# Kernel tuning notes

Hardware: AMD Instinct MI355X
Metric: run time of the kernel (lower is better)

Reference implementation:

```python
import jax, jax.numpy as jnp
import numpy as np
import math

B, S, D_MODEL, N_HEAD, D_HEAD, D_FFN = 1, 2048, 1024, 16, 64, 4096
EPS = 1e-6


def setup_inputs() -> dict:
    key = jax.random.key(0)
    ks = jax.random.split(key, 10)
    scale = 0.02
    x = jax.random.normal(ks[0], (B, S, D_MODEL), dtype=jnp.float32)
    # RoPE frequencies: freqs_cis[s, i] = exp(1j * s * theta_i), theta_i = 10000^{-2i/d_head}
    half = D_HEAD // 2
    inv_freq = 1.0 / (10000.0 ** (jnp.arange(0, half, dtype=jnp.float32) * 2.0 / D_HEAD))
    angles = jnp.arange(S, dtype=jnp.float32)[:, None] * inv_freq[None, :]  # [S, half]
    freqs_cos = jnp.cos(angles)
    freqs_sin = jnp.sin(angles)
    wq = jax.random.normal(ks[1], (D_MODEL, N_HEAD * D_HEAD), dtype=jnp.float32) * scale
    wk = jax.random.normal(ks[2], (D_MODEL, N_HEAD * D_HEAD), dtype=jnp.float32) * scale
    wv = jax.random.normal(ks[3], (D_MODEL, N_HEAD * D_HEAD), dtype=jnp.float32) * scale
    wo = jax.random.normal(ks[4], (N_HEAD * D_HEAD, D_MODEL), dtype=jnp.float32) * scale
    w1 = jax.random.normal(ks[5], (D_MODEL, D_FFN), dtype=jnp.float32) * scale
    w2 = jax.random.normal(ks[6], (D_FFN, D_MODEL), dtype=jnp.float32) * scale
    w3 = jax.random.normal(ks[7], (D_MODEL, D_FFN), dtype=jnp.float32) * scale
    attn_norm_w = jnp.ones((D_MODEL,), dtype=jnp.float32)
    ffn_norm_w = jnp.ones((D_MODEL,), dtype=jnp.float32)
    return {"x": x, "freqs_cos": freqs_cos, "freqs_sin": freqs_sin,
            "wq": wq, "wk": wk, "wv": wv, "wo": wo,
            "w1": w1, "w2": w2, "w3": w3,
            "attn_norm_w": attn_norm_w, "ffn_norm_w": ffn_norm_w}


def _rmsnorm(x, w):
    xf = x.astype(jnp.float32)
    inv = jax.lax.rsqrt(jnp.mean(xf * xf, axis=-1, keepdims=True) + EPS)
    return (xf * inv).astype(x.dtype) * w


def _rope(t, cos, sin):
    # t: [B, S, H, D]; treat last dim as interleaved (even, odd) complex pairs
    b, s, h, d = t.shape
    tr = t.astype(jnp.float32).reshape(b, s, h, d // 2, 2)
    te, to = tr[..., 0], tr[..., 1]
    c = cos[None, :, None, :]
    sn = sin[None, :, None, :]
    out = jnp.stack([te * c - to * sn, te * sn + to * c], axis=-1)
    return out.reshape(b, s, h, d).astype(t.dtype)


def reference(x, freqs_cos, freqs_sin, wq, wk, wv, wo, w1, w2, w3, attn_norm_w, ffn_norm_w):
    bsz, seqlen, _ = x.shape
    # --- attention sub-block ---
    hin = _rmsnorm(x, attn_norm_w)
    q = (hin @ wq).reshape(bsz, seqlen, N_HEAD, D_HEAD)
    k = (hin @ wk).reshape(bsz, seqlen, N_HEAD, D_HEAD)
    v = (hin @ wv).reshape(bsz, seqlen, N_HEAD, D_HEAD)
    q = _rope(q, freqs_cos, freqs_sin)
    k = _rope(k, freqs_cos, freqs_sin)
    # [B, H, S, S] scores, softmax in fp32 (no causal mask in original)
    scores = jnp.einsum('bqhd,bkhd->bhqk', q, k) / math.sqrt(D_HEAD)
    probs = jax.nn.softmax(scores.astype(jnp.float32), axis=-1).astype(q.dtype)
    attn = jnp.einsum('bhqk,bkhd->bqhd', probs, v).reshape(bsz, seqlen, N_HEAD * D_HEAD)
    h = x + attn @ wo
    # --- SwiGLU FFN sub-block ---
    f = _rmsnorm(h, ffn_norm_w)
    ffn = (jax.nn.silu(f @ w1) * (f @ w3)) @ w2
    return h + ffn
```

## Files before the change

kernel.cpp:

```cpp
#include <hip/hip_runtime.h>
#include <stdint.h>
#include <stddef.h>

using bf16x8 = __attribute__((ext_vector_type(8))) __bf16;
using f32x4  = __attribute__((ext_vector_type(4))) float;
using f32x16 = __attribute__((ext_vector_type(16))) float;

__device__ __forceinline__ float bf2f(unsigned short u) {
  union { unsigned int i; float f; } v; v.i = ((unsigned int)u) << 16; return v.f;
}
__device__ __forceinline__ unsigned short f2bf(float f) {
  union { float f; unsigned int i; } v; v.f = f;
  unsigned int r = v.i + 0x7fffu + ((v.i >> 16) & 1u);
  return (unsigned short)(r >> 16);
}
__device__ __forceinline__ unsigned short f2bf_trunc(float f) {
  union { float f; unsigned int i; } v; v.f = f;
  return (unsigned short)(v.i >> 16);
}
__device__ __forceinline__ unsigned int pk_trunc(float a, float b) {
  union { float f; unsigned int i; } x, y; x.f = a; y.f = b;
  return (x.i >> 16) | (y.i & 0xffff0000u);
}
__device__ __forceinline__ bf16x8 mk_bf16x8(unsigned int a, unsigned int b,
                                            unsigned int c, unsigned int d) {
  union { unsigned int u[4]; bf16x8 v; } x;
  x.u[0] = a; x.u[1] = b; x.u[2] = c; x.u[3] = d; return x.v;
}
__device__ __forceinline__ void async16(const void* g, void* l) {
  __builtin_amdgcn_global_load_lds(
      (const __attribute__((address_space(1))) unsigned int*)g,
      (__attribute__((address_space(3))) unsigned int*)l, 16, 0, 0);
}

#define S_LEN 2048
#define DMODEL 1024
#define NHEAD 16
#define DHEAD 64
#define DFFN 4096

struct T4 {
  const float *s0, *s1, *s2, *s3;
  unsigned short *d0, *d1, *d2, *d3;
};
__global__ __launch_bounds__(256) void transpose4_k(T4 j) {
  const float* in = blockIdx.z == 0 ? j.s0 : blockIdx.z == 1 ? j.s1 : blockIdx.z == 2 ? j.s2 : j.s3;
  unsigned short* out = blockIdx.z == 0 ? j.d0 : blockIdx.z == 1 ? j.d1 : blockIdx.z == 2 ? j.d2 : j.d3;
  __shared__ unsigned short tile[32][33];
  const int tx = threadIdx.x & 31;
  const int ty = threadIdx.x >> 5;
  const int bc = blockIdx.x * 32;
  const int br = blockIdx.y * 32;
#pragma unroll
  for (int i = 0; i < 4; ++i)
    tile[ty + i * 8][tx] = f2bf(in[(size_t)(br + ty + i * 8) * 1024 + bc + tx]);
  __syncthreads();
#pragma unroll
  for (int i = 0; i < 4; ++i)
    out[(size_t)(bc + ty + i * 8) * 1024 + br + tx] = tile[tx][ty + i * 8];
}

__global__ __launch_bounds__(256) void transpose13_k(
    const float* __restrict__ w1, const float* __restrict__ w3,
    unsigned short* __restrict__ out) {
  const float* in = blockIdx.z ? w3 : w1;
  const int rb = blockIdx.z * 32;
  __shared__ unsigned short tile[32][33];
  const int tx = threadIdx.x & 31;
  const int ty = threadIdx.x >> 5;
  const int bc = blockIdx.x * 32;
  const int br = blockIdx.y * 32;
#pragma unroll
  for (int i = 0; i < 4; ++i)
    tile[ty + i * 8][tx] = f2bf(in[(size_t)(br + ty + i * 8) * 4096 + bc + tx]);
  __syncthreads();
#pragma unroll
  for (int i = 0; i < 4; ++i) {
    int c = bc + ty + i * 8;
    int dest = (c >> 5) * 64 + rb + (c & 31);
    out[(size_t)dest * 1024 + br + tx] = tile[tx][ty + i * 8];
  }
}

__global__ __launch_bounds__(256) void transpose_w2_k(
    const float* __restrict__ in, unsigned short* __restrict__ out) {
  __shared__ unsigned short tile[32][33];
  const int tx = threadIdx.x & 31;
  const int ty = threadIdx.x >> 5;
  const int bc = blockIdx.x * 32;
  const int br = blockIdx.y * 32;
#pragma unroll
  for (int i = 0; i < 4; ++i)
    tile[ty + i * 8][tx] = f2bf(in[(size_t)(br + ty + i * 8) * 1024 + bc + tx]);
  __syncthreads();
#pragma unroll
  for (int i = 0; i < 4; ++i)
    out[(size_t)(bc + ty + i * 8) * 4096 + br + tx] = tile[tx][ty + i * 8];
}

__global__ __launch_bounds__(256) void vtrans_k(
    const unsigned short* __restrict__ QKV, unsigned short* __restrict__ VtG) {
  __shared__ unsigned short tile[32][33];
  const int tx = threadIdx.x & 31;
  const int ty = threadIdx.x >> 5;
  const int bc = blockIdx.x * 32;
  const int br = blockIdx.y * 32;
#pragma unroll
  for (int i = 0; i < 4; ++i)
    tile[ty + i * 8][tx] = QKV[(size_t)(br + ty + i * 8) * 3072 + 2048 + bc + tx];
  __syncthreads();
#pragma unroll
  for (int i = 0; i < 4; ++i)
    VtG[(size_t)(bc + ty + i * 8) * 2048 + br + tx] = tile[tx][ty + i * 8];
}

__global__ __launch_bounds__(256) void rmsnorm_k(
    const float* __restrict__ X, const float* __restrict__ W,
    unsigned short* __restrict__ Y) {
  const int row = blockIdx.x;
  const int t = threadIdx.x;
  const int lane = t & 63, w = t >> 6;
  const float* x = X + (size_t)row * DMODEL;
  float xs[4];
  float s = 0.f;
#pragma unroll
  for (int i = 0; i < 4; ++i) {
    xs[i] = x[t * 4 + i];
    s += xs[i] * xs[i];
  }
#pragma unroll
  for (int m = 1; m < 64; m <<= 1) s += __shfl_xor(s, m, 64);
  __shared__ float red[4];
  if (lane == 0) red[w] = s;
  __syncthreads();
  float tot = red[0] + red[1] + red[2] + red[3];
  float inv = rsqrtf(tot * (1.0f / DMODEL) + 1e-6f);
#pragma unroll
  for (int i = 0; i < 4; ++i)
    Y[(size_t)row * DMODEL + t * 4 + i] = f2bf(xs[i] * inv * W[t * 4 + i]);
}

template <int MODE>
__global__ __launch_bounds__(256) void gemm_bt(
    const unsigned short* __restrict__ A, int lda,
    const unsigned short* __restrict__ BT,
    void* __restrict__ Cout,
    int K, int N) {
  __shared__ unsigned short As[128 * 64];
  __shared__ unsigned short Bs[128 * 64];
  const int t = threadIdx.x;
  const int lane = t & 63;
  const int w = t >> 6;
  const int qr = (w >> 1) * 64, qc = (w & 1) * 64;
  const int l31 = lane & 31, half = lane >> 5;
  const int m0 = blockIdx.y * 128, n0 = blockIdx.x * 128;

  f32x16 acc[2][2] = {};

  int srow[4], scol[4];
#pragma unroll
  for (int p = 0; p < 4; ++p) {
    int off = p * 2048 + t * 8;
    int r = off >> 6;
    srow[p] = r;
    scol[p] = ((((off >> 3) & 7) ^ (r & 7) ^ ((r >> 3) & 3))) * 8;
  }
  const int gsw = (l31 & 7) ^ (l31 >> 3);

  for (int k0 = 0; k0 < K; k0 += 64) {
    __syncthreads();
#pragma unroll
    for (int p = 0; p < 4; ++p) {
      int off = p * 2048 + t * 8;
      async16(A + (size_t)(m0 + srow[p]) * lda + (k0 + scol[p]), &As[off]);
      async16(BT + (size_t)(n0 + srow[p]) * K + (k0 + scol[p]), &Bs[off]);
    }
    __syncthreads();
#pragma unroll
    for (int ks = 0; ks < 4; ++ks) {
      const int ch = ((ks * 2 + half) ^ gsw) * 8;
      bf16x8 a0 = *(const bf16x8*)&As[(qr + l31) * 64 + ch];
      bf16x8 a1 = *(const bf16x8*)&As[(qr + 32 + l31) * 64 + ch];
      bf16x8 b0 = *(const bf16x8*)&Bs[(qc + l31) * 64 + ch];
      bf16x8 b1 = *(const bf16x8*)&Bs[(qc + 32 + l31) * 64 + ch];
      acc[0][0] = __builtin_amdgcn_mfma_f32_32x32x16_bf16(a0, b0, acc[0][0], 0, 0, 0);
      acc[0][1] = __builtin_amdgcn_mfma_f32_32x32x16_bf16(a0, b1, acc[0][1], 0, 0, 0);
      acc[1][0] = __builtin_amdgcn_mfma_f32_32x32x16_bf16(a1, b0, acc[1][0], 0, 0, 0);
      acc[1][1] = __builtin_amdgcn_mfma_f32_32x32x16_bf16(a1, b1, acc[1][1], 0, 0, 0);
    }
  }

  {
    unsigned short* C = (unsigned short*)Cout;
#pragma unroll
    for (int rt = 0; rt < 2; ++rt)
#pragma unroll
      for (int ct = 0; ct < 2; ++ct)
#pragma unroll
        for (int reg = 0; reg < 16; ++reg) {
          int rr = m0 + qr + rt * 32 + (reg & 3) + 8 * (reg >> 2) + 4 * half;
          int cc = n0 + qc + ct * 32 + l31;
          C[(size_t)rr * N + cc] = f2bf(acc[rt][ct][reg]);
        }
  }
}

__device__ __forceinline__ void mfma8(f32x16& c0, f32x16& c1,
                                      const bf16x8 (&a)[2][4],
                                      const bf16x8 (&b)[4]) {
  __builtin_amdgcn_s_setprio(1);
#pragma unroll
  for (int ks = 0; ks < 4; ++ks) {
    c0 = __builtin_amdgcn_mfma_f32_32x32x16_bf16(a[0][ks], b[ks], c0, 0, 0, 0);
    c1 = __builtin_amdgcn_mfma_f32_32x32x16_bf16(a[1][ks], b[ks], c1, 0, 0, 0);
  }
  __builtin_amdgcn_s_setprio(0);
}

__global__ __launch_bounds__(512, 2) void gemm256_silu(
    const unsigned short* __restrict__ A,
    const unsigned short* __restrict__ BT,
    unsigned short* __restrict__ F) {
  __shared__ unsigned short lds[65536];
  const int t = threadIdx.x;
  const int l = t & 63, l31 = l & 31, half = l >> 5;
  const int w = t >> 6;
  const int wm = w >> 2, wn = w & 3;

  const int orig = blockIdx.x;
  const int bx = (orig & 7) * 4 + ((orig >> 3) & 3);
  const int by = orig >> 5;
  const int m0 = by * 256, n0 = bx * 256;

  const int rA = t >> 3;
  const int sc = ((t & 7) ^ ((t >> 3) & 7) ^ ((t >> 6) & 3)) * 8;
  const int lo = t * 8;

#define STAGE_A(h, tile, d)                                                    \
  { async16(A + (size_t)(m0 + (h) * 128 + rA) * 1024 + (tile) * 64 + sc,       \
            &lds[(d) * 32768 + (h) * 8192 + lo]);                              \
    async16(A + (size_t)(m0 + (h) * 128 + 64 + rA) * 1024 + (tile) * 64 + sc,  \
            &lds[(d) * 32768 + (h) * 8192 + 4096 + lo]); }
#define STAGE_B(h, tile, d)                                                    \
  { async16(BT + (size_t)(n0 + (h) * 128 + rA) * 1024 + (tile) * 64 + sc,      \
            &lds[(d) * 32768 + 16384 + (h) * 8192 + lo]);                      \
    async16(BT + (size_t)(n0 + (h) * 128 + 64 + rA) * 1024 + (tile) * 64 + sc, \
            &lds[(d) * 32768 + 16384 + (h) * 8192 + 4096 + lo]); }

  const int arow = wm * 128 + l31;
  const int brow = wn * 64 + l31;
  const int gsw = (l31 & 7) ^ (l31 >> 3);
  int kc[4];
#pragma unroll
  for (int ks = 0; ks < 4; ++ks) kc[ks] = ((ks * 2 + half) ^ gsw) * 8;

#define LDA(d, mt, ks) (*(const bf16x8*)&lds[(d) * 32768 + (arow + (mt) * 32) * 64 + kc[ks]])
#define LDB(d, nt, ks) (*(const bf16x8*)&lds[(d) * 32768 + 16384 + (brow + (nt) * 32) * 64 + kc[ks]])

  f32x16 acc[4][2] = {};
  bf16x8 afr[2][4], bfr[2][4];

  STAGE_A(0, 0, 0); STAGE_A(1, 0, 0); STAGE_B(0, 0, 0); STAGE_B(1, 0, 0);
  STAGE_A(0, 1, 1); STAGE_A(1, 1, 1);
  asm volatile("s_waitcnt vmcnt(4)" ::: "memory");
  __builtin_amdgcn_s_barrier();

#pragma unroll 1
  for (int i = 0; i < 8; ++i) {
    const int t1 = 2 * i + 1, t2 = 2 * i + 2, t3 = 2 * i + 3;
    const bool more = i < 7;

#pragma unroll
    for (int ks = 0; ks < 4; ++ks) {
      afr[0][ks] = LDA(0, 0, ks);
      afr[1][ks] = LDA(0, 1, ks);
      bfr[0][ks] = LDB(0, 0, ks);
    }
    STAGE_B(0, t1, 1);
    __builtin_amdgcn_s_barrier();
    mfma8(acc[0][0], acc[1][0], afr, bfr[0]);
    __builtin_amdgcn_s_barrier();

#pragma unroll
    for (int ks = 0; ks < 4; ++ks) bfr[1][ks] = LDB(0, 1, ks);
    STAGE_B(1, t1, 1);
    __builtin_amdgcn_s_barrier();
    mfma8(acc[0][1], acc[1][1], afr, bfr[1]);
    __builtin_amdgcn_s_barrier();

#pragma unroll
    for (int ks = 0; ks < 4; ++ks) {
      afr[0][ks] = LDA(0, 2, ks);
      afr[1][ks] = LDA(0, 3, ks);
    }
    if (more) STAGE_B(0, t2, 0);
    __builtin_amdgcn_s_barrier();
    mfma8(acc[2][1], acc[3][1], afr, bfr[1]);
    __builtin_amdgcn_s_barrier();

    if (more) {
      STAGE_B(1, t2, 0);
      STAGE_A(0, t2, 0);
      asm volatile("s_waitcnt vmcnt(8)" ::: "memory");
    } else {
      asm volatile("s_waitcnt vmcnt(2)" ::: "memory");
    }
    __builtin_amdgcn_s_barrier();
    mfma8(acc[2][0], acc[3][0], afr, bfr[0]);
    __builtin_amdgcn_s_barrier();

#pragma unroll
    for (int ks = 0; ks < 4; ++ks) {
      afr[0][ks] = LDA(1, 0, ks);
      afr[1][ks] = LDA(1, 1, ks);
      bfr[0][ks] = LDB(1, 0, ks);
    }
    if (more) {
      STAGE_A(1, t2, 0);
      asm volatile("s_waitcnt vmcnt(8)" ::: "memory");
    } else {
      asm volatile("s_waitcnt vmcnt(0)" ::: "memory");
    }
    __builtin_amdgcn_s_barrier();
    mfma8(acc[0][0], acc[1][0], afr, bfr[0]);
    __builtin_amdgcn_s_barrier();

#pragma unroll
    for (int ks = 0; ks < 4; ++ks) bfr[1][ks] = LDB(1, 1, ks);
    __builtin_amdgcn_s_barrier();
    mfma8(acc[0][1], acc[1][1], afr, bfr[1]);
    __builtin_amdgcn_s_barrier();

#pragma unroll
    for (int ks = 0; ks < 4; ++ks) {
      afr[0][ks] = LDA(1, 2, ks);
      afr[1][ks] = LDA(1, 3, ks);
    }
    __builtin_amdgcn_s_barrier();
    mfma8(acc[2][1], acc[3][1], afr, bfr[1]);
    __builtin_amdgcn_s_barrier();

    if (more) {
      STAGE_A(0, t3, 1);
      STAGE_A(1, t3, 1);
      asm volatile("s_waitcnt vmcnt(4)" ::: "memory");
    } else {
      asm volatile("s_waitcnt vmcnt(0)" ::: "memory");
    }
    __builtin_amdgcn_s_barrier();
    mfma8(acc[2][0], acc[3][0], afr, bfr[0]);
    __builtin_amdgcn_s_barrier();
  }

#undef STAGE_A
#undef STAGE_B
#undef LDA
#undef LDB

  const int ccol = (n0 >> 1) + wn * 32 + l31;
  const int rbase = m0 + wm * 128 + 4 * half;
#pragma unroll
  for (int mt = 0; mt < 4; ++mt)
#pragma unroll
    for (int reg = 0; reg < 16; ++reg) {
      int rr = rbase + mt * 32 + (reg & 3) + 8 * (reg >> 2);
      float a1v = acc[mt][0][reg];
      float a3v = acc[mt][1][reg];
      float f = a1v / (1.f + __expf(-a1v)) * a3v;
      F[(size_t)rr * 4096 + ccol] = f2bf(f);
    }
}

struct PtrPair { float* p0; float* p1; };

__global__ __launch_bounds__(256) void gemm_bt_sk(
    const unsigned short* __restrict__ A, int lda,
    const unsigned short* __restrict__ BT,
    PtrPair parts, int Kc, int Ktot, int N) {
  __shared__ unsigned short As[64 * 64];
  __shared__ unsigned short Bs[128 * 64];
  const int t = threadIdx.x;
  const int lane = t & 63;
  const int w = t >> 6;
  const int qr = (w >> 1) * 32, qc = (w & 1) * 64;
  const int l31 = lane & 31, half = lane >> 5;
  const int m0 = blockIdx.y * 64, n0 = blockIdx.x * 128;
  const int kb = blockIdx.z * Kc;
  const int gsw = (l31 & 7) ^ (l31 >> 3);

  f32x16 acc[2] = {};

  for (int k0 = 0; k0 < Kc; k0 += 64) {
    __syncthreads();
#pragma unroll
    for (int p = 0; p < 2; ++p) {
      int off = p * 2048 + t * 8;
      int r = off >> 6;
      int sc = (((off >> 3) & 7) ^ (r & 7) ^ ((r >> 3) & 3)) * 8;
      async16(A + (size_t)(m0 + r) * lda + (kb + k0 + sc), &As[off]);
    }
#pragma unroll
    for (int p = 0; p < 4; ++p) {
      int off = p * 2048 + t * 8;
      int r = off >> 6;
      int sc = (((off >> 3) & 7) ^ (r & 7) ^ ((r >> 3) & 3)) * 8;
      async16(BT + (size_t)(n0 + r) * Ktot + (kb + k0 + sc), &Bs[off]);
    }
    __syncthreads();
#pragma unroll
    for (int ks = 0; ks < 4; ++ks) {
      const int ch = ((ks * 2 + half) ^ gsw) * 8;
      bf16x8 a0 = *(const bf16x8*)&As[(qr + l31) * 64 + ch];
      bf16x8 b0 = *(const bf16x8*)&Bs[(qc + l31) * 64 + ch];
      bf16x8 b1 = *(const bf16x8*)&Bs[(qc + 32 + l31) * 64 + ch];
      acc[0] = __builtin_amdgcn_mfma_f32_32x32x16_bf16(a0, b0, acc[0], 0, 0, 0);
      acc[1] = __builtin_amdgcn_mfma_f32_32x32x16_bf16(a0, b1, acc[1], 0, 0, 0);
    }
  }

  float* C = blockIdx.z ? parts.p1 : parts.p0;
#pragma unroll
  for (int ct = 0; ct < 2; ++ct)
#pragma unroll
    for (int reg = 0; reg < 16; ++reg) {
      int rr = m0 + qr + (reg & 3) + 8 * (reg >> 2) + 4 * half;
      int cc = n0 + qc + ct * 32 + l31;
      C[(size_t)rr * N + cc] = acc[ct][reg];
    }
}

__global__ __launch_bounds__(256) void reduce2_k(
    const float4* __restrict__ P0, const float4* __restrict__ P1,
    const float4* __restrict__ R, float4* __restrict__ Out, int nvec) {
  int i = blockIdx.x * 256 + threadIdx.x;
  if (i >= nvec) return;
  float4 a = P0[i], b = P1[i], r = R[i];
  float4 o;
  o.x = a.x + b.x + r.x;
  o.y = a.y + b.y + r.y;
  o.z = a.z + b.z + r.z;
  o.w = a.w + b.w + r.w;
  Out[i] = o;
}

__global__ __launch_bounds__(256) void rope_k(
    unsigned short* __restrict__ QKV,
    const float* __restrict__ cosp,
    const float* __restrict__ sinp) {
  int idx = blockIdx.x * 256 + threadIdx.x;
  int s = idx >> 9;
  int rem = idx & 511;
  int h = rem >> 5;
  int i = rem & 31;
  float c = cosp[s * 32 + i];
  float sn = sinp[s * 32 + i];
  size_t off = (size_t)s * 3072 + h * 64 + 2 * i;
  {
    float e = bf2f(QKV[off]), o = bf2f(QKV[off + 1]);
    QKV[off] = f2bf(e * c - o * sn);
    QKV[off + 1] = f2bf(e * sn + o * c);
  }
  {
    float e = bf2f(QKV[off + 1024]), o = bf2f(QKV[off + 1025]);
    QKV[off + 1024] = f2bf((e * c - o * sn) * 0.125f);
    QKV[off + 1025] = f2bf((e * sn + o * c) * 0.125f);
  }
}

__global__ __launch_bounds__(256) void attn_k(
    const unsigned short* __restrict__ QKV,
    const unsigned short* __restrict__ VtG,
    float* __restrict__ O0, float* __restrict__ O1,
    float* __restrict__ L) {
  const int h = blockIdx.y;
  const int qb = blockIdx.x;
  const int z = blockIdx.z;
  const int t = threadIdx.x;
  const int lane = t & 63;
  const int l31 = lane & 31, half = lane >> 5;
  const int w = t >> 6;
  const int q0 = qb * 128 + w * 32;
  const int kbase = z * 1024;
  const int gsw = (l31 & 7) ^ (l31 >> 3);

  __shared__ unsigned short Kt[2][64 * 64];
  __shared__ unsigned short Vt[2][64 * 64];

  const unsigned short* Kp = QKV + 1024 + h * 64;
  const unsigned short* Vg = VtG + (size_t)h * 64 * 2048;

  bf16x8 qf[4];
#pragma unroll
  for (int ks = 0; ks < 4; ++ks)
    qf[ks] = *(const bf16x8*)(QKV + (size_t)(q0 + l31) * 3072 + h * 64 + ks * 16 + half * 8);

#pragma unroll
  for (int p = 0; p < 2; ++p) {
    int off = p * 2048 + t * 8;
    int r = off >> 6;
    int sc8 = (((off >> 3) & 7) ^ (r & 7) ^ ((r >> 3) & 3)) * 8;
    async16(Kp + (size_t)(kbase + r) * 3072 + sc8, &Kt[0][off]);
    async16(Vg + (size_t)r * 2048 + kbase + sc8, &Vt[0][off]);
  }
  asm volatile("s_waitcnt vmcnt(0)" ::: "memory");
  __syncthreads();

  f32x16 oacc[2] = {};
  float l_r = 0.f;

#pragma unroll 1
  for (int kt = 0; kt < 16; ++kt) {
    const int cur = kt & 1;
    if (kt + 1 < 16) {
      int kb2 = kbase + (kt + 1) * 64;
#pragma unroll
      for (int p = 0; p < 2; ++p) {
        int off = p * 2048 + t * 8;
        int r = off >> 6;
        int sc8 = (((off >> 3) & 7) ^ (r & 7) ^ ((r >> 3) & 3)) * 8;
        async16(Kp + (size_t)(kb2 + r) * 3072 + sc8, &Kt[cur ^ 1][off]);
        async16(Vg + (size_t)r * 2048 + kb2 + sc8, &Vt[cur ^ 1][off]);
      }
    }

    f32x16 st[2] = {};
#pragma unroll
    for (int ks = 0; ks < 4; ++ks) {
      const int ch = ((2 * ks + half) ^ gsw) * 8;
      bf16x8 k0 = *(const bf16x8*)&Kt[cur][l31 * 64 + ch];
      bf16x8 k1 = *(const bf16x8*)&Kt[cur][(32 + l31) * 64 + ch];
      st[0] = __builtin_amdgcn_mfma_f32_32x32x16_bf16(k0, qf[ks], st[0], 0, 0, 0);
      st[1] = __builtin_amdgcn_mfma_f32_32x32x16_bf16(k1, qf[ks], st[1], 0, 0, 0);
    }

    float psum = 0.f;
#pragma unroll
    for (int b = 0; b < 2; ++b)
#pragma unroll
      for (int r = 0; r < 16; ++r) {
        float e = __expf(st[b][r]);
        st[b][r] = e;
        psum += e;
      }
    l_r += psum;

    unsigned int pklo[8], pkhi[8];
#pragma unroll
    for (int b = 0; b < 2; ++b)
#pragma unroll
      for (int m = 0; m < 4; ++m) {
        pklo[b * 4 + m] = pk_trunc(st[b][4 * m + 0], st[b][4 * m + 1]);
        pkhi[b * 4 + m] = pk_trunc(st[b][4 * m + 2], st[b][4 * m + 3]);
      }

#pragma unroll
    for (int ks = 0; ks < 4; ++ks) {
      unsigned int keep_lo = half ? pklo[2 * ks + 1] : pklo[2 * ks];
      unsigned int keep_hi = half ? pkhi[2 * ks + 1] : pkhi[2 * ks];
      unsigned int pass_lo = half ? pklo[2 * ks] : pklo[2 * ks + 1];
      unsigned int pass_hi = half ? pkhi[2 * ks] : pkhi[2 * ks + 1];
      unsigned int olo = (unsigned int)__shfl_xor((int)pass_lo, 32, 64);
      unsigned int ohi = (unsigned int)__shfl_xor((int)pass_hi, 32, 64);
      unsigned int w0 = half ? olo : keep_lo;
      unsigned int w1 = half ? ohi : keep_hi;
      unsigned int w2 = half ? keep_lo : olo;
      unsigned int w3 = half ? keep_hi : ohi;
      bf16x8 af = mk_bf16x8(w0, w1, w2, w3);
      const int ch = ((2 * ks + half) ^ gsw) * 8;
      bf16x8 v0 = *(const bf16x8*)&Vt[cur][l31 * 64 + ch];
      bf16x8 v1 = *(const bf16x8*)&Vt[cur][(32 + l31) * 64 + ch];
      oacc[0] = __builtin_amdgcn_mfma_f32_32x32x16_bf16(af, v0, oacc[0], 0, 0, 0);
      oacc[1] = __builtin_amdgcn_mfma_f32_32x32x16_bf16(af, v1, oacc[1], 0, 0, 0);
    }

    __syncthreads();
  }

  float lt = l_r + __shfl_xor(l_r, 32, 64);
  float* Op = z ? O1 : O0;
#pragma unroll
  for (int db = 0; db < 2; ++db)
#pragma unroll
    for (int reg = 0; reg < 16; ++reg) {
      int q = (reg & 3) + 8 * (reg >> 2) + 4 * half;
      Op[(size_t)(q0 + q) * DMODEL + h * 64 + db * 32 + l31] = oacc[db][reg];
    }
  if (half == 0)
    L[(size_t)(h * 2 + z) * S_LEN + q0 + l31] = lt;
}

__global__ __launch_bounds__(256) void attn_combine_k(
    const float4* __restrict__ O0, const float4* __restrict__ O1,
    const float* __restrict__ L, unsigned short* __restrict__ Attn) {
  int i = blockIdx.x * 256 + threadIdx.x;
  int e0 = i * 4;
  int s = e0 >> 10;
  int c = e0 & 1023;
  int h = c >> 6;
  float la = L[(size_t)(h * 2) * S_LEN + s];
  float lb = L[(size_t)(h * 2 + 1) * S_LEN + s];
  float inv = 1.f / (la + lb);
  float4 a = O0[i], b = O1[i];
  ushort4 r;
  r.x = f2bf((a.x + b.x) * inv);
  r.y = f2bf((a.y + b.y) * inv);
  r.z = f2bf((a.z + b.z) * inv);
  r.w = f2bf((a.w + b.w) * inv);
  *(ushort4*)(Attn + e0) = r;
}

extern "C" void kernel_launch(void* const* d_in, const int* in_sizes, int n_in,
                              void* d_out, int out_size, void* d_ws, size_t ws_size,
                              hipStream_t stream) {
  (void)in_sizes; (void)n_in; (void)out_size; (void)ws_size;
  const float* x    = (const float*)d_in[0];
  const float* fcos = (const float*)d_in[1];
  const float* fsin = (const float*)d_in[2];
  const float* wq   = (const float*)d_in[3];
  const float* wk   = (const float*)d_in[4];
  const float* wv   = (const float*)d_in[5];
  const float* wo   = (const float*)d_in[6];
  const float* w1   = (const float*)d_in[7];
  const float* w2   = (const float*)d_in[8];
  const float* w3   = (const float*)d_in[9];
  const float* anw  = (const float*)d_in[10];
  const float* fnw  = (const float*)d_in[11];
  float* out = (float*)d_out;
  char* ws = (char*)d_ws;

  unsigned short* WqkvT = (unsigned short*)(ws + 0);
  unsigned short* VtG   = (unsigned short*)(ws + 0);
  float*          Lbuf  = (float*)(ws + 4194304);
  unsigned short* WoT   = (unsigned short*)(ws + 6291456);
  unsigned short* QKV   = (unsigned short*)(ws + 8388608);
  unsigned short* Attn  = (unsigned short*)(ws + 20971520);
  float* Oa             = (float*)(ws + 25165824);
  float* Ob             = (float*)(ws + 37748736);
  float* P0a            = (float*)(ws + 8388608);
  float* P1a            = (float*)(ws + 25165824);
  unsigned short* F     = (unsigned short*)(ws + 0);
  float* P0b            = (float*)(ws + 16777216);
  float* P1b            = (float*)(ws + 25165824);
  unsigned short* Hin   = (unsigned short*)(ws + 33554432);
  float*          Hres  = (float*)        (ws + 37748736);
  unsigned short* W13I  = (unsigned short*)(ws + 46137344);
  unsigned short* W2T   = (unsigned short*)(ws + 62914560);

  transpose4_k<<<dim3(32, 32, 4), 256, 0, stream>>>(
      T4{wq, wk, wv, wo, WqkvT, WqkvT + 1048576, WqkvT + 2097152, WoT});
  transpose13_k<<<dim3(128, 32, 2), 256, 0, stream>>>(w1, w3, W13I);
  transpose_w2_k<<<dim3(32, 128), 256, 0, stream>>>(w2, W2T);

  rmsnorm_k<<<2048, 256, 0, stream>>>(x, anw, Hin);
  gemm_bt<0><<<dim3(24, 16), 256, 0, stream>>>(Hin, 1024, WqkvT, QKV, 1024, 3072);
  rope_k<<<4096, 256, 0, stream>>>(QKV, fcos, fsin);
  vtrans_k<<<dim3(32, 64), 256, 0, stream>>>(QKV, VtG);
  attn_k<<<dim3(16, 16, 2), 256, 0, stream>>>(QKV, VtG, Oa, Ob, Lbuf);
  attn_combine_k<<<2048, 256, 0, stream>>>((const float4*)Oa, (const float4*)Ob, Lbuf, Attn);
  gemm_bt_sk<<<dim3(8, 32, 2), 256, 0, stream>>>(Attn, 1024, WoT, PtrPair{P0a, P1a}, 512, 1024, 1024);
  reduce2_k<<<2048, 256, 0, stream>>>((const float4*)P0a, (const float4*)P1a,
                                      (const float4*)x, (float4*)Hres, 524288);

  rmsnorm_k<<<2048, 256, 0, stream>>>(Hres, fnw, Hin);
  gemm256_silu<<<dim3(256), 512, 0, stream>>>(Hin, W13I, F);
  gemm_bt_sk<<<dim3(8, 32, 2), 256, 0, stream>>>(F, 4096, W2T, PtrPair{P0b, P1b}, 2048, 4096, 1024);
  reduce2_k<<<2048, 256, 0, stream>>>((const float4*)P0b, (const float4*)P1b,
                                      (const float4*)Hres, (float4*)out, 524288);
}
```

Measured before the change: 295.6 us.

## Enlarge split-K GEMM tiles, vectorize transposes, simplify SiLU GEMM LDS swizzle

The split-K GEMM for the output and down projections moves from 64x128 to 128x128 tiles with four MFMAs per wave per k-step, and its swizzle offsets are hoisted out of the loop. This raises operand reuse but halves the block count. The weight and V transposes use 64x64 tiles with float4 loads and ushort4 stores to cut memory transactions. The SiLU GEMM swizzle is simplified to a plain XOR with the row's low bits on both the stage and read sides.

Measured after the change: 298.9 us. About the same (+1.1%).

```diff
diff --git a/kernel.cpp b/kernel.cpp
--- a/kernel.cpp
+++ b/kernel.cpp
@@ -46,18 +46,32 @@
 __global__ __launch_bounds__(256) void transpose4_k(T4 j) {
   const float* in = blockIdx.z == 0 ? j.s0 : blockIdx.z == 1 ? j.s1 : blockIdx.z == 2 ? j.s2 : j.s3;
   unsigned short* out = blockIdx.z == 0 ? j.d0 : blockIdx.z == 1 ? j.d1 : blockIdx.z == 2 ? j.d2 : j.d3;
-  __shared__ unsigned short tile[32][33];
-  const int tx = threadIdx.x & 31;
-  const int ty = threadIdx.x >> 5;
-  const int bc = blockIdx.x * 32;
-  const int br = blockIdx.y * 32;
-#pragma unroll
-  for (int i = 0; i < 4; ++i)
-    tile[ty + i * 8][tx] = f2bf(in[(size_t)(br + ty + i * 8) * 1024 + bc + tx]);
+  __shared__ unsigned short tile[64][66];
+  const int t = threadIdx.x;
+  const int br = blockIdx.y * 64, bc = blockIdx.x * 64;
+  const int r = t >> 4, c4 = (t & 15) * 4;
+#pragma unroll
+  for (int i = 0; i < 4; ++i) {
+    int row = r + i * 16;
+    float4 v = *(const float4*)&in[(size_t)(br + row) * 1024 + bc + c4];
+    tile[row][c4 + 0] = f2bf(v.x);
+    tile[row][c4 + 1] = f2bf(v.y);
+    tile[row][c4 + 2] = f2bf(v.z);
+    tile[row][c4 + 3] = f2bf(v.w);
+  }
   __syncthreads();
-#pragma unroll
-  for (int i = 0; i < 4; ++i)
-    out[(size_t)(bc + ty + i * 8) * 1024 + br + tx] = tile[tx][ty + i * 8];
+  const int x = t >> 2, y16 = (t & 3) * 16;
+#pragma unroll
+  for (int i = 0; i < 2; ++i) {
+    int y0 = y16 + i * 8;
+    ushort4 o0, o1;
+    o0.x = tile[y0 + 0][x]; o0.y = tile[y0 + 1][x];
+    o0.z = tile[y0 + 2][x]; o0.w = tile[y0 + 3][x];
+    o1.x = tile[y0 + 4][x]; o1.y = tile[y0 + 5][x];
+    o1.z = tile[y0 + 6][x]; o1.w = tile[y0 + 7][x];
+    *(ushort4*)&out[(size_t)(bc + x) * 1024 + br + y0] = o0;
+    *(ushort4*)&out[(size_t)(bc + x) * 1024 + br + y0 + 4] = o1;
+  }
 }
 
 __global__ __launch_bounds__(256) void transpose13_k(
@@ -65,53 +79,93 @@
     unsigned short* __restrict__ out) {
   const float* in = blockIdx.z ? w3 : w1;
   const int rb = blockIdx.z * 32;
-  __shared__ unsigned short tile[32][33];
-  const int tx = threadIdx.x & 31;
-  const int ty = threadIdx.x >> 5;
-  const int bc = blockIdx.x * 32;
-  const int br = blockIdx.y * 32;
-#pragma unroll
-  for (int i = 0; i < 4; ++i)
-    tile[ty + i * 8][tx] = f2bf(in[(size_t)(br + ty + i * 8) * 4096 + bc + tx]);
+  __shared__ unsigned short tile[64][66];
+  const int t = threadIdx.x;
+  const int br = blockIdx.y * 64, bc = blockIdx.x * 64;
+  const int r = t >> 4, c4 = (t & 15) * 4;
+#pragma unroll
+  for (int i = 0; i < 4; ++i) {
+    int row = r + i * 16;
+    float4 v = *(const float4*)&in[(size_t)(br + row) * 4096 + bc + c4];
+    tile[row][c4 + 0] = f2bf(v.x);
+    tile[row][c4 + 1] = f2bf(v.y);
+    tile[row][c4 + 2] = f2bf(v.z);
+    tile[row][c4 + 3] = f2bf(v.w);
+  }
   __syncthreads();
-#pragma unroll
-  for (int i = 0; i < 4; ++i) {
-    int c = bc + ty + i * 8;
-    int dest = (c >> 5) * 64 + rb + (c & 31);
-    out[(size_t)dest * 1024 + br + tx] = tile[tx][ty + i * 8];
+  const int x = t >> 2, y16 = (t & 3) * 16;
+  const int dest = (bc >> 5) * 64 + (x >> 5) * 64 + rb + (x & 31);
+#pragma unroll
+  for (int i = 0; i < 2; ++i) {
+    int y0 = y16 + i * 8;
+    ushort4 o0, o1;
+    o0.x = tile[y0 + 0][x]; o0.y = tile[y0 + 1][x];
+    o0.z = tile[y0 + 2][x]; o0.w = tile[y0 + 3][x];
+    o1.x = tile[y0 + 4][x]; o1.y = tile[y0 + 5][x];
+    o1.z = tile[y0 + 6][x]; o1.w = tile[y0 + 7][x];
+    *(ushort4*)&out[(size_t)dest * 1024 + br + y0] = o0;
+    *(ushort4*)&out[(size_t)dest * 1024 + br + y0 + 4] = o1;
   }
 }
 
 __global__ __launch_bounds__(256) void transpose_w2_k(
     const float* __restrict__ in, unsigned short* __restrict__ out) {
-  __shared__ unsigned short tile[32][33];
-  const int tx = threadIdx.x & 31;
-  const int ty = threadIdx.x >> 5;
-  const int bc = blockIdx.x * 32;
-  const int br = blockIdx.y * 32;
-#pragma unroll
-  for (int i = 0; i < 4; ++i)
-    tile[ty + i * 8][tx] = f2bf(in[(size_t)(br + ty + i * 8) * 1024 + bc + tx]);
+  __shared__ unsigned short tile[64][66];
+  const int t = threadIdx.x;
+  const int br = blockIdx.y * 64, bc = blockIdx.x * 64;
+  const int r = t >> 4, c4 = (t & 15) * 4;
+#pragma unroll
+  for (int i = 0; i < 4; ++i) {
+    int row = r + i * 16;
+    float4 v = *(const float4*)&in[(size_t)(br + row) * 1024 + bc + c4];
+    tile[row][c4 + 0] = f2bf(v.x);
+    tile[row][c4 + 1] = f2bf(v.y);
+    tile[row][c4 + 2] = f2bf(v.z);
+    tile[row][c4 + 3] = f2bf(v.w);
+  }
   __syncthreads();
-#pragma unroll
-  for (int i = 0; i < 4; ++i)
-    out[(size_t)(bc + ty + i * 8) * 4096 + br + tx] = tile[tx][ty + i * 8];
+  const int x = t >> 2, y16 = (t & 3) * 16;
+#pragma unroll
+  for (int i = 0; i < 2; ++i) {
+    int y0 = y16 + i * 8;
+    ushort4 o0, o1;
+    o0.x = tile[y0 + 0][x]; o0.y = tile[y0 + 1][x];
+    o0.z = tile[y0 + 2][x]; o0.w = tile[y0 + 3][x];
+    o1.x = tile[y0 + 4][x]; o1.y = tile[y0 + 5][x];
+    o1.z = tile[y0 + 6][x]; o1.w = tile[y0 + 7][x];
+    *(ushort4*)&out[(size_t)(bc + x) * 4096 + br + y0] = o0;
+    *(ushort4*)&out[(size_t)(bc + x) * 4096 + br + y0 + 4] = o1;
+  }
 }
 
 __global__ __launch_bounds__(256) void vtrans_k(
     const unsigned short* __restrict__ QKV, unsigned short* __restrict__ VtG) {
-  __shared__ unsigned short tile[32][33];
-  const int tx = threadIdx.x & 31;
-  const int ty = threadIdx.x >> 5;
-  const int bc = blockIdx.x * 32;
-  const int br = blockIdx.y * 32;
-#pragma unroll
-  for (int i = 0; i < 4; ++i)
-    tile[ty + i * 8][tx] = QKV[(size_t)(br + ty + i * 8) * 3072 + 2048 + bc + tx];
+  __shared__ unsigned short tile[64][66];
+  const int t = threadIdx.x;
+  const int br = blockIdx.y * 64, bc = blockIdx.x * 64;
+  const int r = t >> 4, c4 = (t & 15) * 4;
+#pragma unroll
+  for (int i = 0; i < 4; ++i) {
+    int row = r + i * 16;
+    ushort4 v = *(const ushort4*)&QKV[(size_t)(br + row) * 3072 + 2048 + bc + c4];
+    tile[row][c4 + 0] = v.x;
+    tile[row][c4 + 1] = v.y;
+    tile[row][c4 + 2] = v.z;
+    tile[row][c4 + 3] = v.w;
+  }
   __syncthreads();
-#pragma unroll
-  for (int i = 0; i < 4; ++i)
-    VtG[(size_t)(bc + ty + i * 8) * 2048 + br + tx] = tile[tx][ty + i * 8];
+  const int x = t >> 2, y16 = (t & 3) * 16;
+#pragma unroll
+  for (int i = 0; i < 2; ++i) {
+    int y0 = y16 + i * 8;
+    ushort4 o0, o1;
+    o0.x = tile[y0 + 0][x]; o0.y = tile[y0 + 1][x];
+    o0.z = tile[y0 + 2][x]; o0.w = tile[y0 + 3][x];
+    o1.x = tile[y0 + 4][x]; o1.y = tile[y0 + 5][x];
+    o1.z = tile[y0 + 6][x]; o1.w = tile[y0 + 7][x];
+    *(ushort4*)&VtG[(size_t)(bc + x) * 2048 + br + y0] = o0;
+    *(ushort4*)&VtG[(size_t)(bc + x) * 2048 + br + y0 + 4] = o1;
+  }
 }
 
 __global__ __launch_bounds__(256) void rmsnorm_k(
@@ -233,7 +287,7 @@
   const int m0 = by * 256, n0 = bx * 256;
 
   const int rA = t >> 3;
-  const int sc = ((t & 7) ^ ((t >> 3) & 7) ^ ((t >> 6) & 3)) * 8;
+  const int sc = ((t & 7) ^ ((t >> 3) & 7)) * 8;
   const int lo = t * 8;
 
 #define STAGE_A(h, tile, d)                                                    \
@@ -249,10 +303,9 @@
 
   const int arow = wm * 128 + l31;
   const int brow = wn * 64 + l31;
-  const int gsw = (l31 & 7) ^ (l31 >> 3);
   int kc[4];
 #pragma unroll
-  for (int ks = 0; ks < 4; ++ks) kc[ks] = ((ks * 2 + half) ^ gsw) * 8;
+  for (int ks = 0; ks < 4; ++ks) kc[ks] = ((ks * 2 + half) ^ (l31 & 7)) * 8;
 
 #define LDA(d, mt, ks) (*(const bf16x8*)&lds[(d) * 32768 + (arow + (mt) * 32) * 64 + kc[ks]])
 #define LDB(d, nt, ks) (*(const bf16x8*)&lds[(d) * 32768 + 16384 + (brow + (nt) * 32) * 64 + kc[ks]])
@@ -373,60 +426,66 @@
 
 struct PtrPair { float* p0; float* p1; };
 
-__global__ __launch_bounds__(256) void gemm_bt_sk(
+__global__ __launch_bounds__(256) void gemm_bt_sk2(
     const unsigned short* __restrict__ A, int lda,
     const unsigned short* __restrict__ BT,
     PtrPair parts, int Kc, int Ktot, int N) {
-  __shared__ unsigned short As[64 * 64];
+  __shared__ unsigned short As[128 * 64];
   __shared__ unsigned short Bs[128 * 64];
   const int t = threadIdx.x;
   const int lane = t & 63;
   const int w = t >> 6;
-  const int qr = (w >> 1) * 32, qc = (w & 1) * 64;
+  const int qr = (w >> 1) * 64, qc = (w & 1) * 64;
   const int l31 = lane & 31, half = lane >> 5;
-  const int m0 = blockIdx.y * 64, n0 = blockIdx.x * 128;
+  const int m0 = blockIdx.y * 128, n0 = blockIdx.x * 128;
   const int kb = blockIdx.z * Kc;
+
+  f32x16 acc[2][2] = {};
+
+  int srow[4], scol[4];
+#pragma unroll
+  for (int p = 0; p < 4; ++p) {
+    int off = p * 2048 + t * 8;
+    int r = off >> 6;
+    srow[p] = r;
+    scol[p] = ((((off >> 3) & 7) ^ (r & 7) ^ ((r >> 3) & 3))) * 8;
+  }
   const int gsw = (l31 & 7) ^ (l31 >> 3);
 
-  f32x16 acc[2] = {};
-
-  for (int k0 = 0; k0 < Kc; k0 += 64) {
+  for (int k0 = kb; k0 < kb + Kc; k0 += 64) {
     __syncthreads();
-#pragma unroll
-    for (int p = 0; p < 2; ++p) {
-      int off = p * 2048 + t * 8;
-      int r = off >> 6;
-      int sc = (((off >> 3) & 7) ^ (r & 7) ^ ((r >> 3) & 3)) * 8;
-      async16(A + (size_t)(m0 + r) * lda + (kb + k0 + sc), &As[off]);
-    }
 #pragma unroll
     for (int p = 0; p < 4; ++p) {
       int off = p * 2048 + t * 8;
-      int r = off >> 6;
-      int sc = (((off >> 3) & 7) ^ (r & 7) ^ ((r >> 3) & 3)) * 8;
-      async16(BT + (size_t)(n0 + r) * Ktot + (kb + k0 + sc), &Bs[off]);
+      async16(A + (size_t)(m0 + srow[p]) * lda + (k0 + scol[p]), &As[off]);
+      async16(BT + (size_t)(n0 + srow[p]) * Ktot + (k0 + scol[p]), &Bs[off]);
     }
     __syncthreads();
 #pragma unroll
     for (int ks = 0; ks < 4; ++ks) {
       const int ch = ((ks * 2 + half) ^ gsw) * 8;
       bf16x8 a0 = *(const bf16x8*)&As[(qr + l31) * 64 + ch];
+      bf16x8 a1 = *(const bf16x8*)&As[(qr + 32 + l31) * 64 + ch];
       bf16x8 b0 = *(const bf16x8*)&Bs[(qc + l31) * 64 + ch];
       bf16x8 b1 = *(const bf16x8*)&Bs[(qc + 32 + l31) * 64 + ch];
-      acc[0] = __builtin_amdgcn_mfma_f32_32x32x16_bf16(a0, b0, acc[0], 0, 0, 0);
-      acc[1] = __builtin_amdgcn_mfma_f32_32x32x16_bf16(a0, b1, acc[1], 0, 0, 0);
+      acc[0][0] = __builtin_amdgcn_mfma_f32_32x32x16_bf16(a0, b0, acc[0][0], 0, 0, 0);
+      acc[0][1] = __builtin_amdgcn_mfma_f32_32x32x16_bf16(a0, b1, acc[0][1], 0, 0, 0);
+      acc[1][0] = __builtin_amdgcn_mfma_f32_32x32x16_bf16(a1, b0, acc[1][0], 0, 0, 0);
+      acc[1][1] = __builtin_amdgcn_mfma_f32_32x32x16_bf16(a1, b1, acc[1][1], 0, 0, 0);
     }
   }
 
   float* C = blockIdx.z ? parts.p1 : parts.p0;
 #pragma unroll
-  for (int ct = 0; ct < 2; ++ct)
-#pragma unroll
-    for (int reg = 0; reg < 16; ++reg) {
-      int rr = m0 + qr + (reg & 3) + 8 * (reg >> 2) + 4 * half;
-      int cc = n0 + qc + ct * 32 + l31;
-      C[(size_t)rr * N + cc] = acc[ct][reg];
-    }
+  for (int rt = 0; rt < 2; ++rt)
+#pragma unroll
+    for (int ct = 0; ct < 2; ++ct)
+#pragma unroll
+      for (int reg = 0; reg < 16; ++reg) {
+        int rr = m0 + qr + rt * 32 + (reg & 3) + 8 * (reg >> 2) + 4 * half;
+        int cc = n0 + qc + ct * 32 + l31;
+        C[(size_t)rr * N + cc] = acc[rt][ct][reg];
+      }
 }
 
 __global__ __launch_bounds__(256) void reduce2_k(
@@ -646,24 +705,24 @@
   unsigned short* W13I  = (unsigned short*)(ws + 46137344);
   unsigned short* W2T   = (unsigned short*)(ws + 62914560);
 
-  transpose4_k<<<dim3(32, 32, 4), 256, 0, stream>>>(
+  transpose4_k<<<dim3(16, 16, 4), 256, 0, stream>>>(
       T4{wq, wk, wv, wo, WqkvT, WqkvT + 1048576, WqkvT + 2097152, WoT});
-  transpose13_k<<<dim3(128, 32, 2), 256, 0, stream>>>(w1, w3, W13I);
-  transpose_w2_k<<<dim3(32, 128), 256, 0, stream>>>(w2, W2T);
+  transpose13_k<<<dim3(64, 16, 2), 256, 0, stream>>>(w1, w3, W13I);
+  transpose_w2_k<<<dim3(16, 64), 256, 0, stream>>>(w2, W2T);
 
   rmsnorm_k<<<2048, 256, 0, stream>>>(x, anw, Hin);
   gemm_bt<0><<<dim3(24, 16), 256, 0, stream>>>(Hin, 1024, WqkvT, QKV, 1024, 3072);
   rope_k<<<4096, 256, 0, stream>>>(QKV, fcos, fsin);
-  vtrans_k<<<dim3(32, 64), 256, 0, stream>>>(QKV, VtG);
+  vtrans_k<<<dim3(16, 32), 256, 0, stream>>>(QKV, VtG);
   attn_k<<<dim3(16, 16, 2), 256, 0, stream>>>(QKV, VtG, Oa, Ob, Lbuf);
   attn_combine_k<<<2048, 256, 0, stream>>>((const float4*)Oa, (const float4*)Ob, Lbuf, Attn);
-  gemm_bt_sk<<<dim3(8, 32, 2), 256, 0, stream>>>(Attn, 1024, WoT, PtrPair{P0a, P1a}, 512, 1024, 1024);
+  gemm_bt_sk2<<<dim3(8, 16, 2), 256, 0, stream>>>(Attn, 1024, WoT, PtrPair{P0a, P1a}, 512, 1024, 1024);
   reduce2_k<<<2048, 256, 0, stream>>>((const float4*)P0a, (const float4*)P1a,
                                       (const float4*)x, (float4*)Hres, 524288);
 
   rmsnorm_k<<<2048, 256, 0, stream>>>(Hres, fnw, Hin);
   gemm256_silu<<<dim3(256), 512, 0, stream>>>(Hin, W13I, F);
-  gemm_bt_sk<<<dim3(8, 32, 2), 256, 0, stream>>>(F, 4096, W2T, PtrPair{P0b, P1b}, 2048, 4096, 1024);
+  gemm_bt_sk2<<<dim3(8, 16, 2), 256, 0, stream>>>(F, 4096, W2T, PtrPair{P0b, P1b}, 2048, 4096, 1024);
   reduce2_k<<<2048, 256, 0, stream>>>((const float4*)P0b, (const float4*)P1b,
                                       (const float4*)Hres, (float4*)out, 524288);
 }
```
